# Kernel tuning notes

Hardware: AMD Instinct MI355X
Metric: run time of the kernel (lower is better)

## Reference

```python
import jax, jax.numpy as jnp
import numpy as np
import math

TAU = 0.05
N_ITERS = 10
LR = 1.0
BETA1 = 0.9
BETA2 = 0.999
EPS_ADAM = 1e-08

BATCH, N, M = 8, 1024, 1024


def setup_inputs() -> dict:
    key = jax.random.key(0)
    log_alpha = jax.random.normal(key, (BATCH, N, M), dtype=jnp.float32)
    return {"log_alpha": log_alpha}


def reference(log_alpha):
    batch, n, m = log_alpha.shape
    dtype = log_alpha.dtype
    # default uniform log-marginals (log_a = -log n, log_b = -log m)
    log_a = jnp.full((batch, n), -math.log(float(n)), dtype=dtype)
    log_b = jnp.full((batch, m), -math.log(float(m)), dtype=dtype)
    # schedule=None -> tau constant, so the kernel is loop-invariant
    kernel = log_alpha / TAU  # [B, N, M]

    def step(carry, iter_idx):
        u, v, m_u, v_u, m_v, v_v = carry
        t = (iter_idx + 1).astype(dtype)
        bc1 = 1.0 - jnp.power(jnp.asarray(BETA1, dtype), t)
        bc2 = 1.0 - jnp.power(jnp.asarray(BETA2, dtype), t)

        # u half-step
        u_target = log_a - jax.nn.logsumexp(kernel + v[:, None, :], axis=-1)
        g_u = u_target - u
        m_u = BETA1 * m_u + (1.0 - BETA1) * g_u
        v_u = BETA2 * v_u + (1.0 - BETA2) * (g_u * g_u)
        u_next = u + LR * (m_u / bc1) / (jnp.sqrt(v_u / bc2) + EPS_ADAM)

        # v half-step (uses u_next, as in the torch loop)
        v_target = log_b - jax.nn.logsumexp(kernel + u_next[:, :, None], axis=-2)
        g_v = v_target - v
        m_v = BETA1 * m_v + (1.0 - BETA1) * g_v
        v_v = BETA2 * v_v + (1.0 - BETA2) * (g_v * g_v)
        v_next = v + LR * (m_v / bc1) / (jnp.sqrt(v_v / bc2) + EPS_ADAM)

        return (u_next, v_next, m_u, v_u, m_v, v_v), None

    z_n = jnp.zeros((batch, n), dtype=dtype)
    z_m = jnp.zeros((batch, m), dtype=dtype)
    init = (z_n, z_m, z_n, z_n, z_m, z_m)
    (u, v, _, _, _, _), _ = jax.lax.scan(step, init, jnp.arange(N_ITERS))

    # final transport plan at the target tau
    plan = jnp.exp(kernel + u[:, :, None] + v[:, None, :])
    return plan
```

## Files before the change

### kernel.cpp

```cpp
#include <hip/hip_runtime.h>
#include <math.h>

#define INV_TAU   20.0f
#define LOGN      6.931471805599453f
#define B1        0.9f
#define B2        0.999f
#define EPS_ADAM  1e-8f

constexpr int BATCH = 8;
constexpr int N = 1024;
constexpr int M = 1024;
constexpr int NCHUNK = 32;
constexpr int ROWS_PER_CHUNK = N / NCHUNK;

__device__ inline float wave_max(float x) {
#pragma unroll
  for (int off = 1; off < 64; off <<= 1) x = fmaxf(x, __shfl_xor(x, off));
  return x;
}
__device__ inline float wave_sum(float x) {
#pragma unroll
  for (int off = 1; off < 64; off <<= 1) x += __shfl_xor(x, off);
  return x;
}

__global__ __launch_bounds__(256) void k_init(float* __restrict__ ws) {
  int i = blockIdx.x * 256 + threadIdx.x;
  ws[i] = 0.0f;
}

__global__ __launch_bounds__(256) void k_row_u(
    const float* __restrict__ la, const float* __restrict__ v,
    float* __restrict__ u, float* __restrict__ mu, float* __restrict__ vu,
    float bc1, float bc2)
{
  int gw   = (blockIdx.x << 2) + (threadIdx.x >> 6);
  int lane = threadIdx.x & 63;
  int b = gw >> 10;
  const float4* rowp = (const float4*)(la + (size_t)gw * M);
  const float4* vp   = (const float4*)(v + b * M);

  float x[16];
  float m = -INFINITY;
#pragma unroll
  for (int t = 0; t < 4; ++t) {
    float4 k4 = rowp[lane + 64 * t];
    float4 v4 = vp[lane + 64 * t];
    x[4*t+0] = fmaf(k4.x, INV_TAU, v4.x);
    x[4*t+1] = fmaf(k4.y, INV_TAU, v4.y);
    x[4*t+2] = fmaf(k4.z, INV_TAU, v4.z);
    x[4*t+3] = fmaf(k4.w, INV_TAU, v4.w);
    m = fmaxf(m, fmaxf(fmaxf(x[4*t+0], x[4*t+1]), fmaxf(x[4*t+2], x[4*t+3])));
  }
  m = wave_max(m);
  float s = 0.0f;
#pragma unroll
  for (int t = 0; t < 16; ++t) s += __expf(x[t] - m);
  s = wave_sum(s);

  if (lane == 0) {
    float lse = m + __logf(s);
    float g   = (-LOGN - lse) - u[gw];
    float mn  = B1 * mu[gw] + (1.0f - B1) * g;
    float vn  = B2 * vu[gw] + (1.0f - B2) * g * g;
    mu[gw] = mn;
    vu[gw] = vn;
    u[gw]  = u[gw] + (mn / bc1) / (sqrtf(vn / bc2) + EPS_ADAM);
  }
}

__global__ __launch_bounds__(256) void k_col_partial(
    const float* __restrict__ la, const float* __restrict__ u,
    float* __restrict__ pm, float* __restrict__ ps)
{
  int b  = blockIdx.x >> 5;
  int cn = blockIdx.x & 31;
  int tid = threadIdx.x;
  int i0 = cn * ROWS_PER_CHUNK;

  __shared__ float su[ROWS_PER_CHUNK];
  if (tid < ROWS_PER_CHUNK) su[tid] = u[b * N + i0 + tid];
  __syncthreads();

  const float4* base = (const float4*)(la + (size_t)(b * N + i0) * M);
  float4 m = make_float4(-INFINITY, -INFINITY, -INFINITY, -INFINITY);
  float4 s = make_float4(0.f, 0.f, 0.f, 0.f);

#pragma unroll 4
  for (int i = 0; i < ROWS_PER_CHUNK; ++i) {
    float uu = su[i];
    float4 k4 = base[i * 256 + tid];
    float x, nm;
    x = fmaf(k4.x, INV_TAU, uu); nm = fmaxf(m.x, x);
    s.x = s.x * __expf(m.x - nm) + __expf(x - nm); m.x = nm;
    x = fmaf(k4.y, INV_TAU, uu); nm = fmaxf(m.y, x);
    s.y = s.y * __expf(m.y - nm) + __expf(x - nm); m.y = nm;
    x = fmaf(k4.z, INV_TAU, uu); nm = fmaxf(m.z, x);
    s.z = s.z * __expf(m.z - nm) + __expf(x - nm); m.z = nm;
    x = fmaf(k4.w, INV_TAU, uu); nm = fmaxf(m.w, x);
    s.w = s.w * __expf(m.w - nm) + __expf(x - nm); m.w = nm;
  }

  int off = cn * (BATCH * M) + b * M;
  ((float4*)(pm + off))[tid] = m;
  ((float4*)(ps + off))[tid] = s;
}

__global__ __launch_bounds__(256) void k_combine_v(
    const float* __restrict__ pm, const float* __restrict__ ps,
    float* __restrict__ v, float* __restrict__ mv, float* __restrict__ vv,
    float bc1, float bc2)
{
  int c = blockIdx.x * 256 + threadIdx.x;
  float Mx = -INFINITY, S = 0.0f;
#pragma unroll
  for (int cn = 0; cn < NCHUNK; ++cn) {
    float m = pm[cn * (BATCH * M) + c];
    float s = ps[cn * (BATCH * M) + c];
    float nM = fmaxf(Mx, m);
    S = S * __expf(Mx - nM) + s * __expf(m - nM);
    Mx = nM;
  }
  float lse = Mx + __logf(S);
  float g  = (-LOGN - lse) - v[c];
  float mn = B1 * mv[c] + (1.0f - B1) * g;
  float vn = B2 * vv[c] + (1.0f - B2) * g * g;
  mv[c] = mn;
  vv[c] = vn;
  v[c]  = v[c] + (mn / bc1) / (sqrtf(vn / bc2) + EPS_ADAM);
}

__global__ __launch_bounds__(256) void k_plan(
    const float* __restrict__ la, const float* __restrict__ u,
    const float* __restrict__ v, float* __restrict__ out)
{
  size_t idx = (size_t)blockIdx.x * 256 + threadIdx.x;
  int row = (int)(idx >> 8);
  int b   = row >> 10;
  int jc  = (int)(idx & 255);
  float ur  = u[row];
  float4 v4 = ((const float4*)(v + b * M))[jc];
  float4 k4 = ((const float4*)la)[idx];
  float4 o;
  o.x = __expf(fmaf(k4.x, INV_TAU, ur + v4.x));
  o.y = __expf(fmaf(k4.y, INV_TAU, ur + v4.y));
  o.z = __expf(fmaf(k4.z, INV_TAU, ur + v4.z));
  o.w = __expf(fmaf(k4.w, INV_TAU, ur + v4.w));
  ((float4*)out)[idx] = o;
}

extern "C" void kernel_launch(void* const* d_in, const int* in_sizes, int n_in,
                              void* d_out, int out_size, void* d_ws, size_t ws_size,
                              hipStream_t stream) {
  const float* la = (const float*)d_in[0];
  float* out = (float*)d_out;
  float* ws  = (float*)d_ws;

  float* u  = ws;
  float* v  = ws + 8192;
  float* mu = ws + 16384;
  float* vu = ws + 24576;
  float* mv = ws + 32768;
  float* vv = ws + 40960;
  float* pm = ws + 49152;
  float* ps = pm + NCHUNK * BATCH * M;

  k_init<<<192, 256, 0, stream>>>(ws);

  for (int it = 0; it < 10; ++it) {
    float t = (float)(it + 1);
    float bc1 = 1.0f - powf(B1, t);
    float bc2 = 1.0f - powf(B2, t);
    k_row_u<<<(BATCH * N) / 4, 256, 0, stream>>>(la, v, u, mu, vu, bc1, bc2);
    k_col_partial<<<BATCH * NCHUNK, 256, 0, stream>>>(la, u, pm, ps);
    k_combine_v<<<(BATCH * M) / 256, 256, 0, stream>>>(pm, ps, v, mv, vv, bc1, bc2);
  }
  k_plan<<<(BATCH * N * M) / 4 / 256, 256, 0, stream>>>(la, u, v, out);
}
```

Before: 275.3 us.

## Fuse Sinkhorn-Adam iterations into one persistent cooperative kernel with register-resident tiles

Replaces the per-iteration launches (row LSE, column partial, combine) and the final plan kernel with one cooperative kernel of 256 blocks. Each block owns 32 rows of one batch. It keeps its scaled log_alpha tile in registers so the column log-sum-exp and the final exp reuse it without re-reading global memory. The row pass still re-reads rows each iteration, and the Adam states for u and v live in shared memory. Grid-wide syncs replace the kernel boundaries; this adds sync cost and high register pressure, and the old multi-kernel path is kept as a fallback if the cooperative launch fails.

```diff
diff --git a/kernel.cpp b/kernel.cpp
--- a/kernel.cpp
+++ b/kernel.cpp
@@ -1,5 +1,8 @@
 #include <hip/hip_runtime.h>
+#include <hip/hip_cooperative_groups.h>
 #include <math.h>
+
+namespace cg = cooperative_groups;
 
 #define INV_TAU   20.0f
 #define LOGN      6.931471805599453f
@@ -10,19 +13,183 @@
 constexpr int BATCH = 8;
 constexpr int N = 1024;
 constexpr int M = 1024;
-constexpr int NCHUNK = 32;
-constexpr int ROWS_PER_CHUNK = N / NCHUNK;
-
-__device__ inline float wave_max(float x) {
+constexpr int NITER = 10;
+
+constexpr int P_RPB  = 32;
+constexpr int P_NCH  = N / P_RPB;
+constexpr int P_NBLK = BATCH * P_NCH;
+constexpr int P_NTHR = 512;
+
+__device__ inline float wave_max64(float x) {
 #pragma unroll
   for (int off = 1; off < 64; off <<= 1) x = fmaxf(x, __shfl_xor(x, off));
   return x;
 }
-__device__ inline float wave_sum(float x) {
+__device__ inline float wave_sum64(float x) {
 #pragma unroll
   for (int off = 1; off < 64; off <<= 1) x += __shfl_xor(x, off);
   return x;
 }
+__device__ inline float2 lse_merge(float2 a, float2 b) {
+  float m = fmaxf(a.x, b.x);
+  float s = a.y * __expf(a.x - m) + b.y * __expf(b.x - m);
+  return make_float2(m, s);
+}
+
+__global__ __launch_bounds__(P_NTHR, 2) void k_sink(
+    const float* __restrict__ la, float* __restrict__ out,
+    float* __restrict__ vg, float* __restrict__ pm, float* __restrict__ ps)
+{
+  cg::grid_group grid = cg::this_grid();
+
+  __shared__ float4 cmm4[256], css4[256];
+  __shared__ float u_s[P_RPB], mu_s[P_RPB], vu_s[P_RPB];
+  __shared__ float vst[P_RPB], mv_s[P_RPB], vv_s[P_RPB];
+
+  const int blk = blockIdx.x;
+  const int b   = blk & 7;
+  const int c   = blk >> 3;
+  const int i0  = c * P_RPB;
+  const int tid = threadIdx.x;
+
+  const float4* la4 = (const float4*)la;
+  const float4* vg4 = (const float4*)(vg + b * M);
+
+  const int c4 = tid & 255;
+  const int rg = tid >> 8;
+  const int w    = tid >> 6;
+  const int lane = tid & 63;
+
+  float4 y[16];
+#pragma unroll
+  for (int rr = 0; rr < 16; ++rr) {
+    float4 t = la4[((size_t)(b * N + i0 + (rg << 4) + rr) << 8) + c4];
+    t.x *= INV_TAU; t.y *= INV_TAU; t.z *= INV_TAU; t.w *= INV_TAU;
+    y[rr] = t;
+  }
+  if (tid < P_RPB) {
+    u_s[tid] = 0.f; mu_s[tid] = 0.f; vu_s[tid] = 0.f;
+    vst[tid] = 0.f; mv_s[tid] = 0.f; vv_s[tid] = 0.f;
+  }
+  __syncthreads();
+
+  float p1 = 1.0f, p2 = 1.0f;
+
+  for (int it = 0; it < NITER; ++it) {
+    p1 *= B1; p2 *= B2;
+    const float bc1 = 1.0f - p1, bc2 = 1.0f - p2;
+
+    for (int s = 0; s < 4; ++s) {
+      const int r = (w << 2) | s;
+      const float4* rowp = la4 + ((size_t)(b * N + i0 + r) << 8);
+      float x[16];
+      float mx = -INFINITY;
+#pragma unroll
+      for (int tq = 0; tq < 4; ++tq) {
+        float4 k4 = rowp[lane + (tq << 6)];
+        float4 v4 = make_float4(0.f, 0.f, 0.f, 0.f);
+        if (it != 0) v4 = vg4[lane + (tq << 6)];
+        x[4*tq+0] = fmaf(k4.x, INV_TAU, v4.x);
+        x[4*tq+1] = fmaf(k4.y, INV_TAU, v4.y);
+        x[4*tq+2] = fmaf(k4.z, INV_TAU, v4.z);
+        x[4*tq+3] = fmaf(k4.w, INV_TAU, v4.w);
+        mx = fmaxf(mx, fmaxf(fmaxf(x[4*tq+0], x[4*tq+1]), fmaxf(x[4*tq+2], x[4*tq+3])));
+      }
+      mx = wave_max64(mx);
+      float ss = 0.f;
+#pragma unroll
+      for (int q = 0; q < 16; ++q) ss += __expf(x[q] - mx);
+      ss = wave_sum64(ss);
+      if (lane == 0) {
+        float lse = mx + __logf(ss);
+        float g   = (-LOGN - lse) - u_s[r];
+        float mn  = B1 * mu_s[r] + (1.0f - B1) * g;
+        float vn  = B2 * vu_s[r] + (1.0f - B2) * g * g;
+        mu_s[r] = mn; vu_s[r] = vn;
+        u_s[r]  = u_s[r] + (mn / bc1) / (sqrtf(vn / bc2) + EPS_ADAM);
+      }
+    }
+    __syncthreads();
+
+    {
+      float4 xm = make_float4(-INFINITY, -INFINITY, -INFINITY, -INFINITY);
+#pragma unroll
+      for (int rr = 0; rr < 16; ++rr) {
+        float uu = u_s[(rg << 4) + rr];
+        xm.x = fmaxf(xm.x, y[rr].x + uu); xm.y = fmaxf(xm.y, y[rr].y + uu);
+        xm.z = fmaxf(xm.z, y[rr].z + uu); xm.w = fmaxf(xm.w, y[rr].w + uu);
+      }
+      float4 xs = make_float4(0.f, 0.f, 0.f, 0.f);
+#pragma unroll
+      for (int rr = 0; rr < 16; ++rr) {
+        float uu = u_s[(rg << 4) + rr];
+        xs.x += __expf(y[rr].x + uu - xm.x); xs.y += __expf(y[rr].y + uu - xm.y);
+        xs.z += __expf(y[rr].z + uu - xm.z); xs.w += __expf(y[rr].w + uu - xm.w);
+      }
+      if (rg == 1) { cmm4[c4] = xm; css4[c4] = xs; }
+      __syncthreads();
+      if (rg == 0) {
+        float4 om = cmm4[c4], os = css4[c4];
+        float4 nm, ns;
+        nm.x = fmaxf(xm.x, om.x); ns.x = xs.x * __expf(xm.x - nm.x) + os.x * __expf(om.x - nm.x);
+        nm.y = fmaxf(xm.y, om.y); ns.y = xs.y * __expf(xm.y - nm.y) + os.y * __expf(om.y - nm.y);
+        nm.z = fmaxf(xm.z, om.z); ns.z = xs.z * __expf(xm.z - nm.z) + os.z * __expf(om.z - nm.z);
+        nm.w = fmaxf(xm.w, om.w); ns.w = xs.w * __expf(xm.w - nm.w) + os.w * __expf(om.w - nm.w);
+        ((float4*)(pm + c * (BATCH * M) + b * M))[c4] = nm;
+        ((float4*)(ps + c * (BATCH * M) + b * M))[c4] = ns;
+      }
+    }
+    grid.sync();
+
+    {
+      const int g2  = tid >> 4;
+      const int l16 = tid & 15;
+      const int j   = i0 + g2;
+      const float* pmp = pm + b * M + j;
+      const float* psp = ps + b * M + j;
+      float2 acc = make_float2(pmp[(size_t)l16 * (BATCH * M)],
+                               psp[(size_t)l16 * (BATCH * M)]);
+      float2 o2  = make_float2(pmp[(size_t)(l16 + 16) * (BATCH * M)],
+                               psp[(size_t)(l16 + 16) * (BATCH * M)]);
+      acc = lse_merge(acc, o2);
+#pragma unroll
+      for (int off = 1; off < 16; off <<= 1) {
+        float om  = __shfl_xor(acc.x, off, 16);
+        float osv = __shfl_xor(acc.y, off, 16);
+        acc = lse_merge(acc, make_float2(om, osv));
+      }
+      if (l16 == 0) {
+        float lse = acc.x + __logf(acc.y);
+        float gv  = (-LOGN - lse) - vst[g2];
+        float mn  = B1 * mv_s[g2] + (1.0f - B1) * gv;
+        float vn  = B2 * vv_s[g2] + (1.0f - B2) * gv * gv;
+        mv_s[g2] = mn; vv_s[g2] = vn;
+        float vnew = vst[g2] + (mn / bc1) / (sqrtf(vn / bc2) + EPS_ADAM);
+        vst[g2] = vnew;
+        vg[b * M + j] = vnew;
+      }
+    }
+    grid.sync();
+  }
+
+  {
+    float4 vv4 = vg4[c4];
+    float4* out4 = (float4*)out;
+#pragma unroll
+    for (int rr = 0; rr < 16; ++rr) {
+      float uu = u_s[(rg << 4) + rr];
+      float4 o;
+      o.x = __expf(y[rr].x + uu + vv4.x);
+      o.y = __expf(y[rr].y + uu + vv4.y);
+      o.z = __expf(y[rr].z + uu + vv4.z);
+      o.w = __expf(y[rr].w + uu + vv4.w);
+      out4[((size_t)(b * N + i0 + (rg << 4) + rr) << 8) + c4] = o;
+    }
+  }
+}
+
+constexpr int F_NCHUNK = 32;
+constexpr int F_RPC    = N / F_NCHUNK;
 
 __global__ __launch_bounds__(256) void k_init(float* __restrict__ ws) {
   int i = blockIdx.x * 256 + threadIdx.x;
@@ -52,11 +219,11 @@
     x[4*t+3] = fmaf(k4.w, INV_TAU, v4.w);
     m = fmaxf(m, fmaxf(fmaxf(x[4*t+0], x[4*t+1]), fmaxf(x[4*t+2], x[4*t+3])));
   }
-  m = wave_max(m);
+  m = wave_max64(m);
   float s = 0.0f;
 #pragma unroll
   for (int t = 0; t < 16; ++t) s += __expf(x[t] - m);
-  s = wave_sum(s);
+  s = wave_sum64(s);
 
   if (lane == 0) {
     float lse = m + __logf(s);
@@ -76,10 +243,10 @@
   int b  = blockIdx.x >> 5;
   int cn = blockIdx.x & 31;
   int tid = threadIdx.x;
-  int i0 = cn * ROWS_PER_CHUNK;
-
-  __shared__ float su[ROWS_PER_CHUNK];
-  if (tid < ROWS_PER_CHUNK) su[tid] = u[b * N + i0 + tid];
+  int i0 = cn * F_RPC;
+
+  __shared__ float su[F_RPC];
+  if (tid < F_RPC) su[tid] = u[b * N + i0 + tid];
   __syncthreads();
 
   const float4* base = (const float4*)(la + (size_t)(b * N + i0) * M);
@@ -87,7 +254,7 @@
   float4 s = make_float4(0.f, 0.f, 0.f, 0.f);
 
 #pragma unroll 4
-  for (int i = 0; i < ROWS_PER_CHUNK; ++i) {
+  for (int i = 0; i < F_RPC; ++i) {
     float uu = su[i];
     float4 k4 = base[i * 256 + tid];
     float x, nm;
@@ -114,7 +281,7 @@
   int c = blockIdx.x * 256 + threadIdx.x;
   float Mx = -INFINITY, S = 0.0f;
 #pragma unroll
-  for (int cn = 0; cn < NCHUNK; ++cn) {
+  for (int cn = 0; cn < F_NCHUNK; ++cn) {
     float m = pm[cn * (BATCH * M) + c];
     float s = ps[cn * (BATCH * M) + c];
     float nM = fmaxf(Mx, m);
@@ -156,24 +323,33 @@
   float* out = (float*)d_out;
   float* ws  = (float*)d_ws;
 
-  float* u  = ws;
-  float* v  = ws + 8192;
-  float* mu = ws + 16384;
-  float* vu = ws + 24576;
-  float* mv = ws + 32768;
-  float* vv = ws + 40960;
-  float* pm = ws + 49152;
-  float* ps = pm + NCHUNK * BATCH * M;
-
-  k_init<<<192, 256, 0, stream>>>(ws);
-
-  for (int it = 0; it < 10; ++it) {
-    float t = (float)(it + 1);
-    float bc1 = 1.0f - powf(B1, t);
-    float bc2 = 1.0f - powf(B2, t);
-    k_row_u<<<(BATCH * N) / 4, 256, 0, stream>>>(la, v, u, mu, vu, bc1, bc2);
-    k_col_partial<<<BATCH * NCHUNK, 256, 0, stream>>>(la, u, pm, ps);
-    k_combine_v<<<(BATCH * M) / 256, 256, 0, stream>>>(pm, ps, v, mv, vv, bc1, bc2);
-  }
-  k_plan<<<(BATCH * N * M) / 4 / 256, 256, 0, stream>>>(la, u, v, out);
-}
+  float* vg = ws;
+  float* pm = ws + BATCH * M;
+  float* ps = pm + P_NCH * BATCH * M;
+
+  void* args[] = { (void*)&la, (void*)&out, (void*)&vg, (void*)&pm, (void*)&ps };
+  hipError_t err = hipLaunchCooperativeKernel((const void*)k_sink,
+                                              dim3(P_NBLK), dim3(P_NTHR),
+                                              args, 0, stream);
+  if (err != hipSuccess) {
+    float* u   = ws;
+    float* v   = ws + 8192;
+    float* mu  = ws + 16384;
+    float* vu  = ws + 24576;
+    float* mv  = ws + 32768;
+    float* vv  = ws + 40960;
+    float* pm2 = ws + 49152;
+    float* ps2 = pm2 + F_NCHUNK * BATCH * M;
+
+    k_init<<<192, 256, 0, stream>>>(ws);
+    for (int it = 0; it < NITER; ++it) {
+      float t = (float)(it + 1);
+      float bc1 = 1.0f - powf(B1, t);
+      float bc2 = 1.0f - powf(B2, t);
+      k_row_u<<<(BATCH * N) / 4, 256, 0, stream>>>(la, v, u, mu, vu, bc1, bc2);
+      k_col_partial<<<BATCH * F_NCHUNK, 256, 0, stream>>>(la, u, pm2, ps2);
+      k_combine_v<<<(BATCH * M) / 256, 256, 0, stream>>>(pm2, ps2, v, mv, vv, bc1, bc2);
+    }
+    k_plan<<<(BATCH * N * M) / 4 / 256, 256, 0, stream>>>(la, u, v, out);
+  }
+}
```

Result: slower. 745.1 us (+170.7%).

## Fuse row-LSE u update and column partial LSE into one kernel per iteration

Applied to the files above, without the earlier changes.

Merges the row logsumexp/Adam u-update kernel with the column partial logsumexp kernel. Each 512-thread block holds a 16-row by 1024-column tile in registers, so log_alpha is read once per iteration instead of twice. Column partials over 64 chunks are combined in a separate kernel that uses four independent accumulators. This costs more registers, several block barriers, and twice as many partial buffers to combine.

```diff
diff --git a/kernel.cpp b/kernel.cpp
--- a/kernel.cpp
+++ b/kernel.cpp
@@ -10,124 +10,162 @@
 constexpr int BATCH = 8;
 constexpr int N = 1024;
 constexpr int M = 1024;
-constexpr int NCHUNK = 32;
-constexpr int ROWS_PER_CHUNK = N / NCHUNK;
-
-__device__ inline float wave_max(float x) {
-#pragma unroll
-  for (int off = 1; off < 64; off <<= 1) x = fmaxf(x, __shfl_xor(x, off));
-  return x;
-}
-__device__ inline float wave_sum(float x) {
-#pragma unroll
-  for (int off = 1; off < 64; off <<= 1) x += __shfl_xor(x, off);
-  return x;
-}
-
-__global__ __launch_bounds__(256) void k_init(float* __restrict__ ws) {
-  int i = blockIdx.x * 256 + threadIdx.x;
-  ws[i] = 0.0f;
-}
-
-__global__ __launch_bounds__(256) void k_row_u(
-    const float* __restrict__ la, const float* __restrict__ v,
+constexpr int NITER = 10;
+constexpr int CHUNKS = 64;
+constexpr int PMSTRIDE = BATCH * M;
+
+__device__ inline float max4f(float4 a) {
+  return fmaxf(fmaxf(a.x, a.y), fmaxf(a.z, a.w));
+}
+
+__global__ __launch_bounds__(256) void k_init(float* __restrict__ p) {
+  p[blockIdx.x * 256 + threadIdx.x] = 0.f;
+}
+
+__global__ __launch_bounds__(512, 4) void k_iter(
+    const float* __restrict__ la, const float* __restrict__ vg,
     float* __restrict__ u, float* __restrict__ mu, float* __restrict__ vu,
+    float* __restrict__ pm, float* __restrict__ ps,
     float bc1, float bc2)
 {
-  int gw   = (blockIdx.x << 2) + (threadIdx.x >> 6);
-  int lane = threadIdx.x & 63;
-  int b = gw >> 10;
-  const float4* rowp = (const float4*)(la + (size_t)gw * M);
-  const float4* vp   = (const float4*)(v + b * M);
-
-  float x[16];
-  float m = -INFINITY;
-#pragma unroll
-  for (int t = 0; t < 4; ++t) {
-    float4 k4 = rowp[lane + 64 * t];
-    float4 v4 = vp[lane + 64 * t];
-    x[4*t+0] = fmaf(k4.x, INV_TAU, v4.x);
-    x[4*t+1] = fmaf(k4.y, INV_TAU, v4.y);
-    x[4*t+2] = fmaf(k4.z, INV_TAU, v4.z);
-    x[4*t+3] = fmaf(k4.w, INV_TAU, v4.w);
-    m = fmaxf(m, fmaxf(fmaxf(x[4*t+0], x[4*t+1]), fmaxf(x[4*t+2], x[4*t+3])));
-  }
-  m = wave_max(m);
-  float s = 0.0f;
-#pragma unroll
-  for (int t = 0; t < 16; ++t) s += __expf(x[t] - m);
-  s = wave_sum(s);
-
+  __shared__ float  wred[16][4];
+  __shared__ float  rowmax[16];
+  __shared__ float  u_s[16];
+  __shared__ float4 cmm4[256], css4[256];
+
+  const int blk = blockIdx.x;
+  const int b   = blk & 7;
+  const int c   = blk >> 3;
+  const int i0  = c * 16;
+  const int tid = threadIdx.x;
+  const int c4  = tid & 255;
+  const int rg  = tid >> 8;
+  const int wq  = (tid >> 6) & 3;
+  const int lane = tid & 63;
+
+  const float4* la4 = (const float4*)la;
+  float4 y[8];
+#pragma unroll
+  for (int rr = 0; rr < 8; ++rr) {
+    float4 t = la4[((size_t)(b * N + i0 + rg * 8 + rr) << 8) + c4];
+    t.x *= INV_TAU; t.y *= INV_TAU; t.z *= INV_TAU; t.w *= INV_TAU;
+    y[rr] = t;
+  }
+  float4 v4 = ((const float4*)(vg + b * M))[c4];
+
+  float rv[8];
+#pragma unroll
+  for (int rr = 0; rr < 8; ++rr) {
+    rv[rr] = max4f(make_float4(y[rr].x + v4.x, y[rr].y + v4.y,
+                               y[rr].z + v4.z, y[rr].w + v4.w));
+  }
+#pragma unroll
+  for (int off = 1; off < 64; off <<= 1) {
+#pragma unroll
+    for (int rr = 0; rr < 8; ++rr) rv[rr] = fmaxf(rv[rr], __shfl_xor(rv[rr], off));
+  }
   if (lane == 0) {
-    float lse = m + __logf(s);
-    float g   = (-LOGN - lse) - u[gw];
-    float mn  = B1 * mu[gw] + (1.0f - B1) * g;
-    float vn  = B2 * vu[gw] + (1.0f - B2) * g * g;
-    mu[gw] = mn;
-    vu[gw] = vn;
-    u[gw]  = u[gw] + (mn / bc1) / (sqrtf(vn / bc2) + EPS_ADAM);
-  }
-}
-
-__global__ __launch_bounds__(256) void k_col_partial(
-    const float* __restrict__ la, const float* __restrict__ u,
-    float* __restrict__ pm, float* __restrict__ ps)
-{
-  int b  = blockIdx.x >> 5;
-  int cn = blockIdx.x & 31;
-  int tid = threadIdx.x;
-  int i0 = cn * ROWS_PER_CHUNK;
-
-  __shared__ float su[ROWS_PER_CHUNK];
-  if (tid < ROWS_PER_CHUNK) su[tid] = u[b * N + i0 + tid];
-  __syncthreads();
-
-  const float4* base = (const float4*)(la + (size_t)(b * N + i0) * M);
-  float4 m = make_float4(-INFINITY, -INFINITY, -INFINITY, -INFINITY);
-  float4 s = make_float4(0.f, 0.f, 0.f, 0.f);
-
-#pragma unroll 4
-  for (int i = 0; i < ROWS_PER_CHUNK; ++i) {
-    float uu = su[i];
-    float4 k4 = base[i * 256 + tid];
-    float x, nm;
-    x = fmaf(k4.x, INV_TAU, uu); nm = fmaxf(m.x, x);
-    s.x = s.x * __expf(m.x - nm) + __expf(x - nm); m.x = nm;
-    x = fmaf(k4.y, INV_TAU, uu); nm = fmaxf(m.y, x);
-    s.y = s.y * __expf(m.y - nm) + __expf(x - nm); m.y = nm;
-    x = fmaf(k4.z, INV_TAU, uu); nm = fmaxf(m.z, x);
-    s.z = s.z * __expf(m.z - nm) + __expf(x - nm); m.z = nm;
-    x = fmaf(k4.w, INV_TAU, uu); nm = fmaxf(m.w, x);
-    s.w = s.w * __expf(m.w - nm) + __expf(x - nm); m.w = nm;
-  }
-
-  int off = cn * (BATCH * M) + b * M;
-  ((float4*)(pm + off))[tid] = m;
-  ((float4*)(ps + off))[tid] = s;
-}
-
-__global__ __launch_bounds__(256) void k_combine_v(
+#pragma unroll
+    for (int rr = 0; rr < 8; ++rr) wred[rg * 8 + rr][wq] = rv[rr];
+  }
+  __syncthreads();
+  if (tid < 16)
+    rowmax[tid] = fmaxf(fmaxf(wred[tid][0], wred[tid][1]),
+                        fmaxf(wred[tid][2], wred[tid][3]));
+  __syncthreads();
+
+#pragma unroll
+  for (int rr = 0; rr < 8; ++rr) {
+    float m = rowmax[rg * 8 + rr];
+    rv[rr] = __expf(y[rr].x + v4.x - m) + __expf(y[rr].y + v4.y - m) +
+             __expf(y[rr].z + v4.z - m) + __expf(y[rr].w + v4.w - m);
+  }
+#pragma unroll
+  for (int off = 1; off < 64; off <<= 1) {
+#pragma unroll
+    for (int rr = 0; rr < 8; ++rr) rv[rr] += __shfl_xor(rv[rr], off);
+  }
+  if (lane == 0) {
+#pragma unroll
+    for (int rr = 0; rr < 8; ++rr) wred[rg * 8 + rr][wq] = rv[rr];
+  }
+  __syncthreads();
+
+  if (tid < 16) {
+    float s   = wred[tid][0] + wred[tid][1] + wred[tid][2] + wred[tid][3];
+    int   gi  = b * N + i0 + tid;
+    float lse = rowmax[tid] + __logf(s);
+    float uo  = u[gi];
+    float g   = (-LOGN - lse) - uo;
+    float mn  = B1 * mu[gi] + (1.0f - B1) * g;
+    float vn  = B2 * vu[gi] + (1.0f - B2) * g * g;
+    mu[gi] = mn; vu[gi] = vn;
+    float un = uo + (mn / bc1) / (sqrtf(vn / bc2) + EPS_ADAM);
+    u[gi] = un; u_s[tid] = un;
+  }
+  __syncthreads();
+
+  float4 xm = make_float4(-INFINITY, -INFINITY, -INFINITY, -INFINITY);
+#pragma unroll
+  for (int rr = 0; rr < 8; ++rr) {
+    float uu = u_s[rg * 8 + rr];
+    xm.x = fmaxf(xm.x, y[rr].x + uu); xm.y = fmaxf(xm.y, y[rr].y + uu);
+    xm.z = fmaxf(xm.z, y[rr].z + uu); xm.w = fmaxf(xm.w, y[rr].w + uu);
+  }
+  float4 xs = make_float4(0.f, 0.f, 0.f, 0.f);
+#pragma unroll
+  for (int rr = 0; rr < 8; ++rr) {
+    float uu = u_s[rg * 8 + rr];
+    xs.x += __expf(y[rr].x + uu - xm.x); xs.y += __expf(y[rr].y + uu - xm.y);
+    xs.z += __expf(y[rr].z + uu - xm.z); xs.w += __expf(y[rr].w + uu - xm.w);
+  }
+  if (rg == 1) { cmm4[c4] = xm; css4[c4] = xs; }
+  __syncthreads();
+  if (rg == 0) {
+    float4 om = cmm4[c4], os = css4[c4], nm, ns;
+    nm.x = fmaxf(xm.x, om.x); ns.x = xs.x * __expf(xm.x - nm.x) + os.x * __expf(om.x - nm.x);
+    nm.y = fmaxf(xm.y, om.y); ns.y = xs.y * __expf(xm.y - nm.y) + os.y * __expf(om.y - nm.y);
+    nm.z = fmaxf(xm.z, om.z); ns.z = xs.z * __expf(xm.z - nm.z) + os.z * __expf(om.z - nm.z);
+    nm.w = fmaxf(xm.w, om.w); ns.w = xs.w * __expf(xm.w - nm.w) + os.w * __expf(om.w - nm.w);
+    ((float4*)(pm + c * PMSTRIDE + b * M))[c4] = nm;
+    ((float4*)(ps + c * PMSTRIDE + b * M))[c4] = ns;
+  }
+}
+
+__global__ __launch_bounds__(256) void k_comb(
     const float* __restrict__ pm, const float* __restrict__ ps,
-    float* __restrict__ v, float* __restrict__ mv, float* __restrict__ vv,
+    float* __restrict__ vg, float* __restrict__ mv, float* __restrict__ vv,
     float bc1, float bc2)
 {
-  int c = blockIdx.x * 256 + threadIdx.x;
-  float Mx = -INFINITY, S = 0.0f;
-#pragma unroll
-  for (int cn = 0; cn < NCHUNK; ++cn) {
-    float m = pm[cn * (BATCH * M) + c];
-    float s = ps[cn * (BATCH * M) + c];
-    float nM = fmaxf(Mx, m);
-    S = S * __expf(Mx - nM) + s * __expf(m - nM);
-    Mx = nM;
-  }
+  const int cx = blockIdx.x * 256 + threadIdx.x;
+  float m0 = -INFINITY, s0 = 0.f, m1 = -INFINITY, s1 = 0.f;
+  float m2 = -INFINITY, s2 = 0.f, m3 = -INFINITY, s3 = 0.f;
+#pragma unroll
+  for (int cn = 0; cn < CHUNKS; cn += 4) {
+    float am, nm;
+    am = pm[(cn + 0) * PMSTRIDE + cx]; nm = fmaxf(m0, am);
+    s0 = s0 * __expf(m0 - nm) + ps[(cn + 0) * PMSTRIDE + cx] * __expf(am - nm); m0 = nm;
+    am = pm[(cn + 1) * PMSTRIDE + cx]; nm = fmaxf(m1, am);
+    s1 = s1 * __expf(m1 - nm) + ps[(cn + 1) * PMSTRIDE + cx] * __expf(am - nm); m1 = nm;
+    am = pm[(cn + 2) * PMSTRIDE + cx]; nm = fmaxf(m2, am);
+    s2 = s2 * __expf(m2 - nm) + ps[(cn + 2) * PMSTRIDE + cx] * __expf(am - nm); m2 = nm;
+    am = pm[(cn + 3) * PMSTRIDE + cx]; nm = fmaxf(m3, am);
+    s3 = s3 * __expf(m3 - nm) + ps[(cn + 3) * PMSTRIDE + cx] * __expf(am - nm); m3 = nm;
+  }
+  float nm01 = fmaxf(m0, m1);
+  float s01  = s0 * __expf(m0 - nm01) + s1 * __expf(m1 - nm01);
+  float nm23 = fmaxf(m2, m3);
+  float s23  = s2 * __expf(m2 - nm23) + s3 * __expf(m3 - nm23);
+  float Mx   = fmaxf(nm01, nm23);
+  float S    = s01 * __expf(nm01 - Mx) + s23 * __expf(nm23 - Mx);
+
   float lse = Mx + __logf(S);
-  float g  = (-LOGN - lse) - v[c];
-  float mn = B1 * mv[c] + (1.0f - B1) * g;
-  float vn = B2 * vv[c] + (1.0f - B2) * g * g;
-  mv[c] = mn;
-  vv[c] = vn;
-  v[c]  = v[c] + (mn / bc1) / (sqrtf(vn / bc2) + EPS_ADAM);
+  float vo  = vg[cx];
+  float g   = (-LOGN - lse) - vo;
+  float mn  = B1 * mv[cx] + (1.0f - B1) * g;
+  float vn  = B2 * vv[cx] + (1.0f - B2) * g * g;
+  mv[cx] = mn; vv[cx] = vn;
+  vg[cx] = vo + (mn / bc1) / (sqrtf(vn / bc2) + EPS_ADAM);
 }
 
 __global__ __launch_bounds__(256) void k_plan(
@@ -163,17 +201,16 @@
   float* mv = ws + 32768;
   float* vv = ws + 40960;
   float* pm = ws + 49152;
-  float* ps = pm + NCHUNK * BATCH * M;
+  float* ps = pm + CHUNKS * PMSTRIDE;
 
   k_init<<<192, 256, 0, stream>>>(ws);
 
-  for (int it = 0; it < 10; ++it) {
+  for (int it = 0; it < NITER; ++it) {
     float t = (float)(it + 1);
     float bc1 = 1.0f - powf(B1, t);
     float bc2 = 1.0f - powf(B2, t);
-    k_row_u<<<(BATCH * N) / 4, 256, 0, stream>>>(la, v, u, mu, vu, bc1, bc2);
-    k_col_partial<<<BATCH * NCHUNK, 256, 0, stream>>>(la, u, pm, ps);
-    k_combine_v<<<(BATCH * M) / 256, 256, 0, stream>>>(pm, ps, v, mv, vv, bc1, bc2);
+    k_iter<<<CHUNKS * BATCH, 512, 0, stream>>>(la, v, u, mu, vu, pm, ps, bc1, bc2);
+    k_comb<<<(BATCH * M) / 256, 256, 0, stream>>>(pm, ps, v, mv, vv, bc1, bc2);
   }
   k_plan<<<(BATCH * N * M) / 4 / 256, 256, 0, stream>>>(la, u, v, out);
 }
```

Result: faster. 255.7 us (-7.1%).
